# Performance work log

Measured on AMD Instinct MI355X. Metric: run time of the kernel, lower is better.

Reference implementation:

```python
import jax, jax.numpy as jnp
import numpy as np

N = 100000      # nodes
E = 1600000     # edges (avg degree 16)
F_N, F_E, H = 5, 3, 64
L = 3           # num GCN layers


def setup_inputs() -> dict:
    key = jax.random.key(0)
    ks = jax.random.split(key, 20)
    s = 0.05
    p = lambda k, shape: jax.random.normal(k, shape, jnp.float32) * s
    return {
        "x": jax.random.normal(ks[0], (N, F_N), jnp.float32),
        "edge_index": jax.random.randint(ks[1], (2, E), 0, N, dtype=jnp.int32),
        "edge_attr": jax.random.normal(ks[2], (E, F_E), jnp.float32),
        # node / edge encoders
        "Wn": p(ks[3], (F_N, H)), "bn": jnp.zeros((H,), jnp.float32),
        "We": p(ks[4], (F_E, H)), "be": jnp.zeros((H,), jnp.float32),
        # stacked GCNConv weights [L, H, H] and biases [L, H]
        "Wc": p(ks[5], (L, H, H)), "bc": jnp.zeros((L, H), jnp.float32),
        # demand forecast head
        "Wd1": p(ks[6], (H, H // 2)), "bd1": jnp.zeros((H // 2,), jnp.float32),
        "Wd2": p(ks[7], (H // 2, 1)), "bd2": jnp.zeros((1,), jnp.float32),
        # inventory optimizer head
        "Wi1": p(ks[8], (H, H // 2)), "bi1": jnp.zeros((H // 2,), jnp.float32),
        "Wi2": p(ks[9], (H // 2, 1)), "bi2": jnp.zeros((1,), jnp.float32),
    }


def reference(x, edge_index, edge_attr, Wn, bn, We, be, Wc, bc,
              Wd1, bd1, Wd2, bd2, Wi1, bi1, Wi2, bi2):
    src, dst = edge_index[0], edge_index[1]
    n = x.shape[0]

    h = jax.nn.relu(x @ Wn + bn)                      # [N, H]
    _ea = jax.nn.relu(edge_attr @ We + be)            # encoded edge feats (GCNConv ignores them)

    # GCN symmetric normalization with self-loops: deg[i] = in_degree(i) + 1
    ones_e = jnp.ones(src.shape[0], h.dtype)
    deg = jax.ops.segment_sum(ones_e, dst, num_segments=n) + 1.0
    dinv = jax.lax.rsqrt(deg)                         # [N]
    norm_e = dinv[src] * dinv[dst]                    # [E]
    norm_self = (dinv * dinv)[:, None]                # [N, 1]

    for l in range(Wc.shape[0]):
        hw = h @ Wc[l]                                # [N, H]
        msgs = norm_e[:, None] * hw[src]              # gather + scale, [E, H]
        agg = jax.ops.segment_sum(msgs, dst, num_segments=n) + norm_self * hw
        h = jax.nn.relu(agg + bc[l])

    demand = jax.nn.relu(h @ Wd1 + bd1) @ Wd2 + bd2   # [N, 1]
    inventory = jax.nn.relu(h @ Wi1 + bi1) @ Wi2 + bi2
    return demand, inventory
```

## Files before the change

### kernel.cpp

```cpp
#include <hip/hip_runtime.h>

#define H 64
#define FN 5
#define EPB 4096
#define BSHIFT 8
#define CAP2 4864

typedef _Float16 half4 __attribute__((ext_vector_type(4)));
typedef _Float16 half8 __attribute__((ext_vector_type(8)));
typedef float    float8v __attribute__((ext_vector_type(8)));

__global__ void k_bscatter2(const int* __restrict__ src, const int* __restrict__ dst,
                            int* __restrict__ lofs_g, int* __restrict__ bcounts,
                            int* __restrict__ binned, int nE, int nbB) {
    __shared__ int lh[512], lpos[512], lcur[512], tmp[256];
    __shared__ int stage[EPB];
    int t = threadIdx.x;
    int e0 = blockIdx.x * EPB;
    int es[16], ed[16];
    lh[t] = 0; lh[t + 256] = 0;
    __syncthreads();
#pragma unroll
    for (int i = 0; i < 16; ++i) {
        int e = e0 + i * 256 + t;
        bool v = e < nE;
        es[i] = v ? src[e] : 0;
        ed[i] = v ? dst[e] : -1;
        if (v) atomicAdd(&lh[ed[i] >> BSHIFT], 1);
    }
    __syncthreads();
    int a0 = lh[2 * t], a1 = lh[2 * t + 1];
    tmp[t] = a0 + a1;
    __syncthreads();
    for (int s = 1; s < 256; s <<= 1) {
        int a = (t >= s) ? tmp[t - s] : 0;
        __syncthreads();
        tmp[t] += a;
        __syncthreads();
    }
    int ex = tmp[t] - (a0 + a1);
    lpos[2 * t] = ex;
    lpos[2 * t + 1] = ex + a0;
    __syncthreads();
    lcur[t] = lpos[t]; lcur[t + 256] = lpos[t + 256];
    size_t row = (size_t)blockIdx.x * (nbB + 1);
    for (int b = t; b <= nbB; b += 256) lofs_g[row + b] = lpos[b];
    for (int b = t; b < nbB; b += 256) if (lh[b]) atomicAdd(&bcounts[b], lh[b]);
    __syncthreads();
#pragma unroll
    for (int i = 0; i < 16; ++i) {
        if (ed[i] >= 0) {
            int b = ed[i] >> BSHIFT;
            int p = atomicAdd(&lcur[b], 1);
            stage[p] = es[i] | ((ed[i] & 255) << 17);
        }
    }
    __syncthreads();
    int total = lpos[nbB];
    for (int j = t; j < total; j += 256) binned[e0 + j] = stage[j];
}

__global__ void k_bscan2(const int* __restrict__ bcounts, int* __restrict__ bbase, int nbB) {
    __shared__ int tmp[512];
    int t = threadIdx.x;
    int v = (t < nbB) ? bcounts[t] : 0;
    tmp[t] = v;
    __syncthreads();
    for (int s = 1; s < 512; s <<= 1) {
        int a = (t >= s) ? tmp[t - s] : 0;
        __syncthreads();
        tmp[t] += a;
        __syncthreads();
    }
    if (t < nbB) bbase[t + 1] = tmp[t];
    if (t == 0) bbase[0] = 0;
}

__global__ void k_bcsr2(const int* __restrict__ binned, const int* __restrict__ lofs_g,
                        const int* __restrict__ bbase, int* __restrict__ row_ptr,
                        int* __restrict__ csr_src, float* __restrict__ dinv,
                        int n, int nE, int nbE, int nbB) {
    __shared__ int len_s[512], start_s[512], roff[512], tmp[256];
    __shared__ int deg[256], st[256], cur[256];
    __shared__ int lbuf[CAP2];
    __shared__ int stage2[CAP2];
    int t = threadIdx.x;
    int B = blockIdx.x;
    int node0 = B << BSHIFT;
    int nn = min(256, n - node0);
    len_s[t] = 0; len_s[t + 256] = 0;
    __syncthreads();
    for (int sb = t; sb < nbE; sb += 256) {
        size_t row = (size_t)sb * (nbB + 1);
        int o0 = lofs_g[row + B], o1 = lofs_g[row + B + 1];
        len_s[sb] = o1 - o0;
        start_s[sb] = sb * EPB + o0;
    }
    __syncthreads();
    int a0 = len_s[2 * t], a1 = len_s[2 * t + 1];
    tmp[t] = a0 + a1;
    __syncthreads();
    for (int s = 1; s < 256; s <<= 1) {
        int a = (t >= s) ? tmp[t - s] : 0;
        __syncthreads();
        tmp[t] += a;
        __syncthreads();
    }
    int ex = tmp[t] - (a0 + a1);
    roff[2 * t] = ex;
    roff[2 * t + 1] = ex + a0;
    __syncthreads();
    int total = min(roff[511] + len_s[511], CAP2);
    for (int sb = t; sb < nbE; sb += 256) {
        int s0 = start_s[sb], ln = len_s[sb], d0 = roff[sb];
        for (int k = 0; k < ln; ++k) {
            int d = d0 + k;
            if (d < CAP2) lbuf[d] = binned[s0 + k];
        }
    }
    deg[t] = 0;
    __syncthreads();
    for (int i = t; i < total; i += 256) atomicAdd(&deg[(lbuf[i] >> 17) & 255], 1);
    __syncthreads();
    tmp[t] = deg[t];
    __syncthreads();
    for (int s = 1; s < 256; s <<= 1) {
        int a = (t >= s) ? tmp[t - s] : 0;
        __syncthreads();
        tmp[t] += a;
        __syncthreads();
    }
    st[t] = tmp[t] - deg[t];
    cur[t] = st[t];
    __syncthreads();
    int base = bbase[B];
    if (t < nn) {
        row_ptr[node0 + t] = base + st[t];
        dinv[node0 + t] = 1.0f / sqrtf((float)deg[t] + 1.0f);
    }
    if (B == 0 && t == 0) row_ptr[n] = nE;
    for (int i = t; i < total; i += 256) {
        int p0 = lbuf[i];
        int p = atomicAdd(&cur[(p0 >> 17) & 255], 1);
        int sv = p0 & 0x1FFFF;
        if (p < CAP2) stage2[p] = sv;
        else csr_src[base + p] = sv;
    }
    __syncthreads();
    for (int i = t; i < total; i += 256) csr_src[base + i] = stage2[i];
}

__global__ void k_enc(const float* __restrict__ x, const float* __restrict__ Wn,
                      const float* __restrict__ bn, const float* __restrict__ dinv,
                      _Float16* __restrict__ g0, int n) {
    int tid = blockIdx.x * 256 + threadIdx.x;
    int node = tid >> 6, ch = tid & 63;
    if (node >= n) return;
    float acc = bn[ch];
#pragma unroll
    for (int k = 0; k < FN; ++k)
        acc += x[(size_t)node * FN + k] * Wn[k * H + ch];
    g0[(size_t)node * H + ch] = (_Float16)(fmaxf(acc, 0.f) * dinv[node]);
}

__global__ void k_layer(const _Float16* __restrict__ gin, const int* __restrict__ csr_src,
                        const int* __restrict__ row_ptr, const float* __restrict__ dinv,
                        const float* __restrict__ W, const float* __restrict__ bias,
                        _Float16* __restrict__ gout, float* __restrict__ hout,
                        int n, int last) {
    __shared__ float As[64 * 68];
    __shared__ int rp_s[65];
    __shared__ float dv_s[64];
    int t = threadIdx.x;
    int wave = t >> 6, lane = t & 63;
    int base = blockIdx.x * 64;
    if (t < 65) rp_s[t] = row_ptr[min(base + t, n)];
    if (t >= 128 && t < 192) {
        int nd = base + (t - 128);
        dv_s[t - 128] = (nd < n) ? dinv[nd] : 0.f;
    }
    __syncthreads();

    int c8 = (lane >> 3) * 8;
    int slot = lane & 7;
    for (int it = 0; it < 8; ++it) {
        int rA = it * 8 + wave, rB = rA + 4;
        int nodeA = base + rA, nodeB = base + rB;
        float8v accA = 0.f, accB = 0.f;
        int iA = rp_s[rA], eA = rp_s[rA + 1];
        int iB = rp_s[rB], eB = rp_s[rB + 1];
        while (iA + 8 <= eA && iB + 8 <= eB) {
            int xA = csr_src[iA + slot];
            int xB = csr_src[iB + slot];
            half8 vA = *(const half8*)(gin + (size_t)xA * H + c8);
            half8 vB = *(const half8*)(gin + (size_t)xB * H + c8);
#pragma unroll
            for (int k = 0; k < 8; ++k) { accA[k] += (float)vA[k]; accB[k] += (float)vB[k]; }
            iA += 8; iB += 8;
        }
        while (iA + 8 <= eA) {
            int xA = csr_src[iA + slot];
            half8 vA = *(const half8*)(gin + (size_t)xA * H + c8);
#pragma unroll
            for (int k = 0; k < 8; ++k) accA[k] += (float)vA[k];
            iA += 8;
        }
        while (iB + 8 <= eB) {
            int xB = csr_src[iB + slot];
            half8 vB = *(const half8*)(gin + (size_t)xB * H + c8);
#pragma unroll
            for (int k = 0; k < 8; ++k) accB[k] += (float)vB[k];
            iB += 8;
        }
        if (iA + slot < eA) {
            int xA = csr_src[iA + slot];
            half8 vA = *(const half8*)(gin + (size_t)xA * H + c8);
#pragma unroll
            for (int k = 0; k < 8; ++k) accA[k] += (float)vA[k];
        }
        if (iB + slot < eB) {
            int xB = csr_src[iB + slot];
            half8 vB = *(const half8*)(gin + (size_t)xB * H + c8);
#pragma unroll
            for (int k = 0; k < 8; ++k) accB[k] += (float)vB[k];
        }
#pragma unroll
        for (int m = 1; m <= 4; m <<= 1) {
#pragma unroll
            for (int k = 0; k < 8; ++k) {
                accA[k] += __shfl_xor(accA[k], m, 64);
                accB[k] += __shfl_xor(accB[k], m, 64);
            }
        }
        if (slot == 0) {
            float oA[8], oB[8];
            if (nodeA < n) {
                half8 sA = *(const half8*)(gin + (size_t)nodeA * H + c8);
                float dA = dv_s[rA];
#pragma unroll
                for (int k = 0; k < 8; ++k) oA[k] = (accA[k] + (float)sA[k]) * dA;
            } else {
#pragma unroll
                for (int k = 0; k < 8; ++k) oA[k] = 0.f;
            }
            if (nodeB < n) {
                half8 sB = *(const half8*)(gin + (size_t)nodeB * H + c8);
                float dB = dv_s[rB];
#pragma unroll
                for (int k = 0; k < 8; ++k) oB[k] = (accB[k] + (float)sB[k]) * dB;
            } else {
#pragma unroll
                for (int k = 0; k < 8; ++k) oB[k] = 0.f;
            }
            *(float4*)&As[rA * 68 + c8]     = make_float4(oA[0], oA[1], oA[2], oA[3]);
            *(float4*)&As[rA * 68 + c8 + 4] = make_float4(oA[4], oA[5], oA[6], oA[7]);
            *(float4*)&As[rB * 68 + c8]     = make_float4(oB[0], oB[1], oB[2], oB[3]);
            *(float4*)&As[rB * 68 + c8 + 4] = make_float4(oB[4], oB[5], oB[6], oB[7]);
        }
    }
    __syncthreads();

    int tx = t & 15, ty = t >> 4;
    int c0 = tx * 4;
    const float* a0 = As + (ty * 4 + 0) * 68;
    const float* a1 = As + (ty * 4 + 1) * 68;
    const float* a2 = As + (ty * 4 + 2) * 68;
    const float* a3 = As + (ty * 4 + 3) * 68;
    float4 acc0 = make_float4(0.f, 0.f, 0.f, 0.f);
    float4 acc1 = acc0, acc2 = acc0, acc3 = acc0;
#pragma unroll 16
    for (int k = 0; k < H; ++k) {
        float4 w = *(const float4*)(W + k * H + c0);
        float v0 = a0[k], v1 = a1[k], v2 = a2[k], v3 = a3[k];
        acc0.x += v0 * w.x; acc0.y += v0 * w.y; acc0.z += v0 * w.z; acc0.w += v0 * w.w;
        acc1.x += v1 * w.x; acc1.y += v1 * w.y; acc1.z += v1 * w.z; acc1.w += v1 * w.w;
        acc2.x += v2 * w.x; acc2.y += v2 * w.y; acc2.z += v2 * w.z; acc2.w += v2 * w.w;
        acc3.x += v3 * w.x; acc3.y += v3 * w.y; acc3.z += v3 * w.z; acc3.w += v3 * w.w;
    }
    float4 b = *(const float4*)(bias + c0);
    float4 accs[4] = {acc0, acc1, acc2, acc3};
#pragma unroll
    for (int rr = 0; rr < 4; ++rr) {
        int r = ty * 4 + rr;
        int row = base + r;
        if (row < n) {
            float4 o;
            o.x = fmaxf(accs[rr].x + b.x, 0.f);
            o.y = fmaxf(accs[rr].y + b.y, 0.f);
            o.z = fmaxf(accs[rr].z + b.z, 0.f);
            o.w = fmaxf(accs[rr].w + b.w, 0.f);
            if (last) {
                *(float4*)(hout + (size_t)row * H + c0) = o;
            } else {
                float d = dv_s[r];
                half4 hh;
                hh.x = (_Float16)(o.x * d);
                hh.y = (_Float16)(o.y * d);
                hh.z = (_Float16)(o.z * d);
                hh.w = (_Float16)(o.w * d);
                *(half4*)(gout + (size_t)row * H + c0) = hh;
            }
        }
    }
}

__global__ void k_heads(const float* __restrict__ h,
                        const float* __restrict__ Wd1, const float* __restrict__ bd1,
                        const float* __restrict__ Wd2, const float* __restrict__ bd2,
                        const float* __restrict__ Wi1, const float* __restrict__ bi1,
                        const float* __restrict__ Wi2, const float* __restrict__ bi2,
                        float* __restrict__ out, int n) {
    __shared__ float hs[64 * 65];
    int lane = threadIdx.x;
    int base = blockIdx.x * 64;
    for (int r = 0; r < 64; ++r) {
        int row = base + r;
        hs[r * 65 + lane] = (row < n) ? h[(size_t)row * H + lane] : 0.f;
    }
    __syncthreads();

    float accd[32], acci[32];
#pragma unroll
    for (int j = 0; j < 32; ++j) { accd[j] = bd1[j]; acci[j] = bi1[j]; }
    for (int k = 0; k < H; ++k) {
        float hk = hs[lane * 65 + k];
#pragma unroll
        for (int j = 0; j < 32; ++j) {
            accd[j] += hk * Wd1[k * 32 + j];
            acci[j] += hk * Wi1[k * 32 + j];
        }
    }
    float demand = bd2[0], inventory = bi2[0];
#pragma unroll
    for (int j = 0; j < 32; ++j) {
        demand    += fmaxf(accd[j], 0.f) * Wd2[j];
        inventory += fmaxf(acci[j], 0.f) * Wi2[j];
    }
    int node = base + lane;
    if (node < n) {
        out[node] = demand;
        out[n + node] = inventory;
    }
}

extern "C" void kernel_launch(void* const* d_in, const int* in_sizes, int n_in,
                              void* d_out, int out_size, void* d_ws, size_t ws_size,
                              hipStream_t stream) {
    const float* x   = (const float*)d_in[0];
    const int*   ei  = (const int*)  d_in[1];
    const float* Wn  = (const float*)d_in[3];
    const float* bn  = (const float*)d_in[4];
    const float* Wc  = (const float*)d_in[7];
    const float* bc  = (const float*)d_in[8];
    const float* Wd1 = (const float*)d_in[9];
    const float* bd1 = (const float*)d_in[10];
    const float* Wd2 = (const float*)d_in[11];
    const float* bd2 = (const float*)d_in[12];
    const float* Wi1 = (const float*)d_in[13];
    const float* bi1 = (const float*)d_in[14];
    const float* Wi2 = (const float*)d_in[15];
    const float* bi2 = (const float*)d_in[16];

    const int n  = in_sizes[0] / FN;
    const int nE = in_sizes[1] / 2;
    const int* src = ei;
    const int* dst = ei + nE;

    const int nbE = (nE + EPB - 1) / EPB;
    const int nbB = (n + 255) >> BSHIFT;
    const int nbL = (n + 63) / 64;

    char* w = (char*)d_ws;
    int* binned    = (int*)w;   w += (size_t)nbE * EPB * 4;
    int* csr_src   = (int*)w;   w += (size_t)nE * 4;
    int* row_ptr   = (int*)w;   w += (size_t)(n + 4) * 4;
    float* dinv    = (float*)w; w += (size_t)n * 4;
    int* lofs      = (int*)w;   w += (size_t)nbE * (nbB + 1) * 4;
    int* bcounts   = (int*)w;   w += 512 * 4;
    int* bbase     = (int*)w;   w += 516 * 4;
    float* hbuf    = (float*)w; w += (size_t)n * H * 4;
    _Float16* gA   = (_Float16*)w; w += (size_t)n * H * 2;
    _Float16* gB   = (_Float16*)w; w += (size_t)n * H * 2;

    hipMemsetAsync(bcounts, 0, 512 * 4, stream);

    k_bscatter2<<<nbE, 256, 0, stream>>>(src, dst, lofs, bcounts, binned, nE, nbB);
    k_bscan2   <<<1,   512, 0, stream>>>(bcounts, bbase, nbB);
    k_bcsr2    <<<nbB, 256, 0, stream>>>(binned, lofs, bbase, row_ptr, csr_src,
                                         dinv, n, nE, nbE, nbB);

    k_enc<<<((size_t)n * 64 + 255) / 256, 256, 0, stream>>>(x, Wn, bn, dinv, gA, n);

    k_layer<<<nbL, 256, 0, stream>>>(gA, csr_src, row_ptr, dinv, Wc,
                                     bc, gB, hbuf, n, 0);
    k_layer<<<nbL, 256, 0, stream>>>(gB, csr_src, row_ptr, dinv, Wc + (size_t)H * H,
                                     bc + H, gA, hbuf, n, 0);
    k_layer<<<nbL, 256, 0, stream>>>(gA, csr_src, row_ptr, dinv, Wc + (size_t)2 * H * H,
                                     bc + 2 * H, gB, hbuf, n, 1);

    k_heads<<<(n + 63) / 64, 64, 0, stream>>>(hbuf, Wd1, bd1, Wd2, bd2,
                                              Wi1, bi1, Wi2, bi2, (float*)d_out, n);
}
```

Measured before the change: 387.7 us.

## Fold bucket scan into CSR build, parallelize run copy, widen layer gather

```diff
diff --git a/kernel.cpp b/kernel.cpp
--- a/kernel.cpp
+++ b/kernel.cpp
@@ -60,44 +60,40 @@
     for (int j = t; j < total; j += 256) binned[e0 + j] = stage[j];
 }
 
-__global__ void k_bscan2(const int* __restrict__ bcounts, int* __restrict__ bbase, int nbB) {
-    __shared__ int tmp[512];
-    int t = threadIdx.x;
-    int v = (t < nbB) ? bcounts[t] : 0;
-    tmp[t] = v;
-    __syncthreads();
-    for (int s = 1; s < 512; s <<= 1) {
-        int a = (t >= s) ? tmp[t - s] : 0;
-        __syncthreads();
-        tmp[t] += a;
-        __syncthreads();
-    }
-    if (t < nbB) bbase[t + 1] = tmp[t];
-    if (t == 0) bbase[0] = 0;
-}
-
 __global__ void k_bcsr2(const int* __restrict__ binned, const int* __restrict__ lofs_g,
-                        const int* __restrict__ bbase, int* __restrict__ row_ptr,
+                        const int* __restrict__ bcounts, int* __restrict__ row_ptr,
                         int* __restrict__ csr_src, float* __restrict__ dinv,
                         int n, int nE, int nbE, int nbB) {
-    __shared__ int len_s[512], start_s[512], roff[512], tmp[256];
+    __shared__ int runlen[512], runstart[512], roff[512], tmp[256];
     __shared__ int deg[256], st[256], cur[256];
+    __shared__ int sh_base, sh_total;
     __shared__ int lbuf[CAP2];
     __shared__ int stage2[CAP2];
     int t = threadIdx.x;
     int B = blockIdx.x;
     int node0 = B << BSHIFT;
     int nn = min(256, n - node0);
-    len_s[t] = 0; len_s[t + 256] = 0;
+
+    int myb = 0;
+    for (int b = t; b < B; b += 256) myb += bcounts[b];
+    tmp[t] = myb;
+    __syncthreads();
+    for (int s = 128; s > 0; s >>= 1) {
+        if (t < s) tmp[t] += tmp[t + s];
+        __syncthreads();
+    }
+    if (t == 0) sh_base = tmp[0];
+
+    runlen[t] = 0; runlen[t + 256] = 0;
     __syncthreads();
     for (int sb = t; sb < nbE; sb += 256) {
         size_t row = (size_t)sb * (nbB + 1);
         int o0 = lofs_g[row + B], o1 = lofs_g[row + B + 1];
-        len_s[sb] = o1 - o0;
-        start_s[sb] = sb * EPB + o0;
-    }
-    __syncthreads();
-    int a0 = len_s[2 * t], a1 = len_s[2 * t + 1];
+        runlen[sb] = o1 - o0;
+        runstart[sb] = sb * EPB + o0;
+    }
+    __syncthreads();
+    int a0 = runlen[2 * t], a1 = runlen[2 * t + 1];
     tmp[t] = a0 + a1;
     __syncthreads();
     for (int s = 1; s < 256; s <<= 1) {
@@ -109,14 +105,17 @@
     int ex = tmp[t] - (a0 + a1);
     roff[2 * t] = ex;
     roff[2 * t + 1] = ex + a0;
-    __syncthreads();
-    int total = min(roff[511] + len_s[511], CAP2);
-    for (int sb = t; sb < nbE; sb += 256) {
-        int s0 = start_s[sb], ln = len_s[sb], d0 = roff[sb];
-        for (int k = 0; k < ln; ++k) {
-            int d = d0 + k;
-            if (d < CAP2) lbuf[d] = binned[s0 + k];
-        }
+    if (t == 255) sh_total = tmp[255];
+    __syncthreads();
+    int total = min(sh_total, CAP2);
+
+    for (int j = t; j < total; j += 256) {
+        int lo = 0, hi = nbE - 1;
+        while (lo < hi) {
+            int mid = (lo + hi + 1) >> 1;
+            if (roff[mid] <= j) lo = mid; else hi = mid - 1;
+        }
+        lbuf[j] = binned[runstart[lo] + (j - roff[lo])];
     }
     deg[t] = 0;
     __syncthreads();
@@ -133,7 +132,7 @@
     st[t] = tmp[t] - deg[t];
     cur[t] = st[t];
     __syncthreads();
-    int base = bbase[B];
+    int base = sh_base;
     if (t < nn) {
         row_ptr[node0 + t] = base + st[t];
         dinv[node0 + t] = 1.0f / sqrtf((float)deg[t] + 1.0f);
@@ -163,143 +162,133 @@
     g0[(size_t)node * H + ch] = (_Float16)(fmaxf(acc, 0.f) * dinv[node]);
 }
 
+__device__ __forceinline__ void drain8(const _Float16* __restrict__ gin,
+                                       const int* __restrict__ cs, int i, int e,
+                                       int slot, int c8, float8v& acc) {
+    while (i + 8 <= e) {
+        int x = cs[i + slot];
+        half8 v = *(const half8*)(gin + (size_t)x * H + c8);
+#pragma unroll
+        for (int k = 0; k < 8; ++k) acc[k] += (float)v[k];
+        i += 8;
+    }
+    if (i + slot < e) {
+        int x = cs[i + slot];
+        half8 v = *(const half8*)(gin + (size_t)x * H + c8);
+#pragma unroll
+        for (int k = 0; k < 8; ++k) acc[k] += (float)v[k];
+    }
+}
+
 __global__ void k_layer(const _Float16* __restrict__ gin, const int* __restrict__ csr_src,
                         const int* __restrict__ row_ptr, const float* __restrict__ dinv,
                         const float* __restrict__ W, const float* __restrict__ bias,
                         _Float16* __restrict__ gout, float* __restrict__ hout,
                         int n, int last) {
-    __shared__ float As[64 * 68];
-    __shared__ int rp_s[65];
-    __shared__ float dv_s[64];
+    __shared__ float As[32 * 68];
+    __shared__ int rp_s[33];
+    __shared__ float dv_s[32];
     int t = threadIdx.x;
     int wave = t >> 6, lane = t & 63;
-    int base = blockIdx.x * 64;
-    if (t < 65) rp_s[t] = row_ptr[min(base + t, n)];
-    if (t >= 128 && t < 192) {
-        int nd = base + (t - 128);
-        dv_s[t - 128] = (nd < n) ? dinv[nd] : 0.f;
+    int base = blockIdx.x * 32;
+    if (t < 33) rp_s[t] = row_ptr[min(base + t, n)];
+    if (t >= 64 && t < 96) {
+        int nd = base + (t - 64);
+        dv_s[t - 64] = (nd < n) ? dinv[nd] : 0.f;
     }
     __syncthreads();
 
     int c8 = (lane >> 3) * 8;
     int slot = lane & 7;
-    for (int it = 0; it < 8; ++it) {
-        int rA = it * 8 + wave, rB = rA + 4;
-        int nodeA = base + rA, nodeB = base + rB;
-        float8v accA = 0.f, accB = 0.f;
-        int iA = rp_s[rA], eA = rp_s[rA + 1];
-        int iB = rp_s[rB], eB = rp_s[rB + 1];
-        while (iA + 8 <= eA && iB + 8 <= eB) {
-            int xA = csr_src[iA + slot];
-            int xB = csr_src[iB + slot];
-            half8 vA = *(const half8*)(gin + (size_t)xA * H + c8);
-            half8 vB = *(const half8*)(gin + (size_t)xB * H + c8);
-#pragma unroll
-            for (int k = 0; k < 8; ++k) { accA[k] += (float)vA[k]; accB[k] += (float)vB[k]; }
-            iA += 8; iB += 8;
-        }
-        while (iA + 8 <= eA) {
-            int xA = csr_src[iA + slot];
-            half8 vA = *(const half8*)(gin + (size_t)xA * H + c8);
-#pragma unroll
-            for (int k = 0; k < 8; ++k) accA[k] += (float)vA[k];
-            iA += 8;
-        }
-        while (iB + 8 <= eB) {
-            int xB = csr_src[iB + slot];
-            half8 vB = *(const half8*)(gin + (size_t)xB * H + c8);
-#pragma unroll
-            for (int k = 0; k < 8; ++k) accB[k] += (float)vB[k];
-            iB += 8;
-        }
-        if (iA + slot < eA) {
-            int xA = csr_src[iA + slot];
-            half8 vA = *(const half8*)(gin + (size_t)xA * H + c8);
-#pragma unroll
-            for (int k = 0; k < 8; ++k) accA[k] += (float)vA[k];
-        }
-        if (iB + slot < eB) {
-            int xB = csr_src[iB + slot];
-            half8 vB = *(const half8*)(gin + (size_t)xB * H + c8);
-#pragma unroll
-            for (int k = 0; k < 8; ++k) accB[k] += (float)vB[k];
-        }
-#pragma unroll
-        for (int m = 1; m <= 4; m <<= 1) {
-#pragma unroll
-            for (int k = 0; k < 8; ++k) {
-                accA[k] += __shfl_xor(accA[k], m, 64);
-                accB[k] += __shfl_xor(accB[k], m, 64);
+    int r0 = wave * 4;
+    int i0 = rp_s[r0],     e0 = rp_s[r0 + 1];
+    int i1 = rp_s[r0 + 1], e1 = rp_s[r0 + 2];
+    int i2 = rp_s[r0 + 2], e2 = rp_s[r0 + 3];
+    int i3 = rp_s[r0 + 3], e3 = rp_s[r0 + 4];
+    float8v acc0 = 0.f, acc1 = 0.f, acc2 = 0.f, acc3 = 0.f;
+    while (i0 + 8 <= e0 && i1 + 8 <= e1 && i2 + 8 <= e2 && i3 + 8 <= e3) {
+        int x0 = csr_src[i0 + slot];
+        int x1 = csr_src[i1 + slot];
+        int x2 = csr_src[i2 + slot];
+        int x3 = csr_src[i3 + slot];
+        half8 v0 = *(const half8*)(gin + (size_t)x0 * H + c8);
+        half8 v1 = *(const half8*)(gin + (size_t)x1 * H + c8);
+        half8 v2 = *(const half8*)(gin + (size_t)x2 * H + c8);
+        half8 v3 = *(const half8*)(gin + (size_t)x3 * H + c8);
+#pragma unroll
+        for (int k = 0; k < 8; ++k) {
+            acc0[k] += (float)v0[k];
+            acc1[k] += (float)v1[k];
+            acc2[k] += (float)v2[k];
+            acc3[k] += (float)v3[k];
+        }
+        i0 += 8; i1 += 8; i2 += 8; i3 += 8;
+    }
+    drain8(gin, csr_src, i0, e0, slot, c8, acc0);
+    drain8(gin, csr_src, i1, e1, slot, c8, acc1);
+    drain8(gin, csr_src, i2, e2, slot, c8, acc2);
+    drain8(gin, csr_src, i3, e3, slot, c8, acc3);
+#pragma unroll
+    for (int m = 1; m <= 4; m <<= 1) {
+#pragma unroll
+        for (int k = 0; k < 8; ++k) {
+            acc0[k] += __shfl_xor(acc0[k], m, 64);
+            acc1[k] += __shfl_xor(acc1[k], m, 64);
+            acc2[k] += __shfl_xor(acc2[k], m, 64);
+            acc3[k] += __shfl_xor(acc3[k], m, 64);
+        }
+    }
+    if (slot == 0) {
+        float8v* accp[4] = {&acc0, &acc1, &acc2, &acc3};
+#pragma unroll
+        for (int s = 0; s < 4; ++s) {
+            int r = r0 + s;
+            int node = base + r;
+            float o[8];
+            if (node < n) {
+                half8 sf = *(const half8*)(gin + (size_t)node * H + c8);
+                float d = dv_s[r];
+                float8v& a = *accp[s];
+#pragma unroll
+                for (int k = 0; k < 8; ++k) o[k] = (a[k] + (float)sf[k]) * d;
+            } else {
+#pragma unroll
+                for (int k = 0; k < 8; ++k) o[k] = 0.f;
             }
-        }
-        if (slot == 0) {
-            float oA[8], oB[8];
-            if (nodeA < n) {
-                half8 sA = *(const half8*)(gin + (size_t)nodeA * H + c8);
-                float dA = dv_s[rA];
-#pragma unroll
-                for (int k = 0; k < 8; ++k) oA[k] = (accA[k] + (float)sA[k]) * dA;
-            } else {
-#pragma unroll
-                for (int k = 0; k < 8; ++k) oA[k] = 0.f;
-            }
-            if (nodeB < n) {
-                half8 sB = *(const half8*)(gin + (size_t)nodeB * H + c8);
-                float dB = dv_s[rB];
-#pragma unroll
-                for (int k = 0; k < 8; ++k) oB[k] = (accB[k] + (float)sB[k]) * dB;
-            } else {
-#pragma unroll
-                for (int k = 0; k < 8; ++k) oB[k] = 0.f;
-            }
-            *(float4*)&As[rA * 68 + c8]     = make_float4(oA[0], oA[1], oA[2], oA[3]);
-            *(float4*)&As[rA * 68 + c8 + 4] = make_float4(oA[4], oA[5], oA[6], oA[7]);
-            *(float4*)&As[rB * 68 + c8]     = make_float4(oB[0], oB[1], oB[2], oB[3]);
-            *(float4*)&As[rB * 68 + c8 + 4] = make_float4(oB[4], oB[5], oB[6], oB[7]);
+            *(float4*)&As[r * 68 + c8]     = make_float4(o[0], o[1], o[2], o[3]);
+            *(float4*)&As[r * 68 + c8 + 4] = make_float4(o[4], o[5], o[6], o[7]);
         }
     }
     __syncthreads();
 
     int tx = t & 15, ty = t >> 4;
     int c0 = tx * 4;
-    const float* a0 = As + (ty * 4 + 0) * 68;
-    const float* a1 = As + (ty * 4 + 1) * 68;
-    const float* a2 = As + (ty * 4 + 2) * 68;
-    const float* a3 = As + (ty * 4 + 3) * 68;
-    float4 acc0 = make_float4(0.f, 0.f, 0.f, 0.f);
-    float4 acc1 = acc0, acc2 = acc0, acc3 = acc0;
+    const float* A0 = As + ty * 68;
+    float4 acc = make_float4(0.f, 0.f, 0.f, 0.f);
 #pragma unroll 16
     for (int k = 0; k < H; ++k) {
         float4 w = *(const float4*)(W + k * H + c0);
-        float v0 = a0[k], v1 = a1[k], v2 = a2[k], v3 = a3[k];
-        acc0.x += v0 * w.x; acc0.y += v0 * w.y; acc0.z += v0 * w.z; acc0.w += v0 * w.w;
-        acc1.x += v1 * w.x; acc1.y += v1 * w.y; acc1.z += v1 * w.z; acc1.w += v1 * w.w;
-        acc2.x += v2 * w.x; acc2.y += v2 * w.y; acc2.z += v2 * w.z; acc2.w += v2 * w.w;
-        acc3.x += v3 * w.x; acc3.y += v3 * w.y; acc3.z += v3 * w.z; acc3.w += v3 * w.w;
+        float v0 = A0[k];
+        acc.x += v0 * w.x; acc.y += v0 * w.y; acc.z += v0 * w.z; acc.w += v0 * w.w;
     }
     float4 b = *(const float4*)(bias + c0);
-    float4 accs[4] = {acc0, acc1, acc2, acc3};
-#pragma unroll
-    for (int rr = 0; rr < 4; ++rr) {
-        int r = ty * 4 + rr;
-        int row = base + r;
-        if (row < n) {
-            float4 o;
-            o.x = fmaxf(accs[rr].x + b.x, 0.f);
-            o.y = fmaxf(accs[rr].y + b.y, 0.f);
-            o.z = fmaxf(accs[rr].z + b.z, 0.f);
-            o.w = fmaxf(accs[rr].w + b.w, 0.f);
-            if (last) {
-                *(float4*)(hout + (size_t)row * H + c0) = o;
-            } else {
-                float d = dv_s[r];
-                half4 hh;
-                hh.x = (_Float16)(o.x * d);
-                hh.y = (_Float16)(o.y * d);
-                hh.z = (_Float16)(o.z * d);
-                hh.w = (_Float16)(o.w * d);
-                *(half4*)(gout + (size_t)row * H + c0) = hh;
-            }
+    int row = base + ty;
+    if (row < n) {
+        float4 o;
+        o.x = fmaxf(acc.x + b.x, 0.f);
+        o.y = fmaxf(acc.y + b.y, 0.f);
+        o.z = fmaxf(acc.z + b.z, 0.f);
+        o.w = fmaxf(acc.w + b.w, 0.f);
+        if (last) {
+            *(float4*)(hout + (size_t)row * H + c0) = o;
+        } else {
+            float d = dv_s[ty];
+            half4 hh;
+            hh.x = (_Float16)(o.x * d);
+            hh.y = (_Float16)(o.y * d);
+            hh.z = (_Float16)(o.z * d);
+            hh.w = (_Float16)(o.w * d);
+            *(half4*)(gout + (size_t)row * H + c0) = hh;
         }
     }
 }
@@ -368,7 +357,7 @@
 
     const int nbE = (nE + EPB - 1) / EPB;
     const int nbB = (n + 255) >> BSHIFT;
-    const int nbL = (n + 63) / 64;
+    const int nbL = (n + 31) / 32;
 
     char* w = (char*)d_ws;
     int* binned    = (int*)w;   w += (size_t)nbE * EPB * 4;
@@ -377,7 +366,6 @@
     float* dinv    = (float*)w; w += (size_t)n * 4;
     int* lofs      = (int*)w;   w += (size_t)nbE * (nbB + 1) * 4;
     int* bcounts   = (int*)w;   w += 512 * 4;
-    int* bbase     = (int*)w;   w += 516 * 4;
     float* hbuf    = (float*)w; w += (size_t)n * H * 4;
     _Float16* gA   = (_Float16*)w; w += (size_t)n * H * 2;
     _Float16* gB   = (_Float16*)w; w += (size_t)n * H * 2;
@@ -385,17 +373,16 @@
     hipMemsetAsync(bcounts, 0, 512 * 4, stream);
 
     k_bscatter2<<<nbE, 256, 0, stream>>>(src, dst, lofs, bcounts, binned, nE, nbB);
-    k_bscan2   <<<1,   512, 0, stream>>>(bcounts, bbase, nbB);
-    k_bcsr2    <<<nbB, 256, 0, stream>>>(binned, lofs, bbase, row_ptr, csr_src,
+    k_bcsr2    <<<nbB, 256, 0, stream>>>(binned, lofs, bcounts, row_ptr, csr_src,
                                          dinv, n, nE, nbE, nbB);
 
     k_enc<<<((size_t)n * 64 + 255) / 256, 256, 0, stream>>>(x, Wn, bn, dinv, gA, n);
 
-    k_layer<<<nbL, 256, 0, stream>>>(gA, csr_src, row_ptr, dinv, Wc,
+    k_layer<<<nbL, 512, 0, stream>>>(gA, csr_src, row_ptr, dinv, Wc,
                                      bc, gB, hbuf, n, 0);
-    k_layer<<<nbL, 256, 0, stream>>>(gB, csr_src, row_ptr, dinv, Wc + (size_t)H * H,
+    k_layer<<<nbL, 512, 0, stream>>>(gB, csr_src, row_ptr, dinv, Wc + (size_t)H * H,
                                      bc + H, gA, hbuf, n, 0);
-    k_layer<<<nbL, 256, 0, stream>>>(gA, csr_src, row_ptr, dinv, Wc + (size_t)2 * H * H,
+    k_layer<<<nbL, 512, 0, stream>>>(gA, csr_src, row_ptr, dinv, Wc + (size_t)2 * H * H,
                                      bc + 2 * H, gB, hbuf, n, 1);
 
     k_heads<<<(n + 63) / 64, 64, 0, stream>>>(hbuf, Wd1, bd1, Wd2, bd2,
```

New measurement: 564.9 us. +45.7%, slower.
